# Optimization experiments

Hardware: AMD Instinct MI355X
Metric: run time of the kernel (lower is better)

The kernel has to match this reference:

```python
import jax, jax.numpy as jnp
import numpy as np

D_MODEL = 1024
NUM_HEADS = 16
D_HEAD = D_MODEL // NUM_HEADS
WINDOW = 512
N_GLOBAL = 1


def longformer_mask(seq_len):
    # sliding window |i-j| <= window//2, plus global rows/cols for first N_GLOBAL tokens
    i = jnp.arange(seq_len)[:, None]
    j = jnp.arange(seq_len)[None, :]
    allowed = (jnp.abs(i - j) <= WINDOW // 2) | (i < N_GLOBAL) | (j < N_GLOBAL)
    return jnp.where(allowed, 0.0, -jnp.inf).astype(jnp.float32)


def setup_inputs() -> dict:
    key = jax.random.key(0)
    ks = jax.random.split(key, 6)
    B, S = 2, 2048
    scale = 1.0 / np.sqrt(D_MODEL)
    return {
        "hidden_states": jax.random.normal(ks[0], (B, S, D_MODEL), dtype=jnp.float32),
        "Wq": jax.random.normal(ks[1], (D_MODEL, D_MODEL), dtype=jnp.float32) * scale,
        "Wk": jax.random.normal(ks[2], (D_MODEL, D_MODEL), dtype=jnp.float32) * scale,
        "Wv": jax.random.normal(ks[3], (D_MODEL, D_MODEL), dtype=jnp.float32) * scale,
        "Wo": jax.random.normal(ks[4], (D_MODEL, D_MODEL), dtype=jnp.float32) * scale,
        "bo": jax.random.normal(ks[5], (D_MODEL,), dtype=jnp.float32) * 0.01,
    }


def reference(hidden_states, Wq, Wk, Wv, Wo, bo):
    B, S, _ = hidden_states.shape
    q = (hidden_states @ Wq).reshape(B, S, NUM_HEADS, D_HEAD).transpose(0, 2, 1, 3)
    k = (hidden_states @ Wk).reshape(B, S, NUM_HEADS, D_HEAD).transpose(0, 2, 1, 3)
    v = (hidden_states @ Wv).reshape(B, S, NUM_HEADS, D_HEAD).transpose(0, 2, 1, 3)
    mask = longformer_mask(S)  # [S, S]
    scores = jnp.einsum('bhqd,bhkd->bhqk', q, k) / np.sqrt(D_HEAD)
    scores = scores + mask[None, None]
    attn = jax.nn.softmax(scores, axis=-1)
    out = jnp.einsum('bhqk,bhkd->bhqd', attn, v)
    out = out.transpose(0, 2, 1, 3).reshape(B, S, D_MODEL)
    return out @ Wo + bo
```

## Files before the change

### kernel.cpp

```cpp
#include <hip/hip_runtime.h>
#include <cstdint>
#include <cstddef>

#define DM 1024
#define NH 16
#define DH 64
#define SEQ 2048
#define NB 2
#define WIN2 256
#define QBLK 64
#define KBLK 128

typedef float f32x4 __attribute__((ext_vector_type(4)));
typedef __bf16 bf16x8 __attribute__((ext_vector_type(8)));
typedef unsigned short u16x8 __attribute__((ext_vector_type(8)));
typedef unsigned short u16x4 __attribute__((ext_vector_type(4)));
typedef float f32x4v __attribute__((ext_vector_type(4)));

__device__ __forceinline__ unsigned short f2bf(float x) {
  unsigned int u = __float_as_uint(x);
  u += 0x7FFFu + ((u >> 16) & 1u);
  return (unsigned short)(u >> 16);
}
__device__ __forceinline__ float bf2f(unsigned short h) {
  return __uint_as_float(((unsigned int)h) << 16);
}
__device__ __forceinline__ f32x4 mfma_bf16(u16x8 a, u16x8 b, f32x4 c) {
  return __builtin_amdgcn_mfma_f32_16x16x32_bf16(
      __builtin_bit_cast(bf16x8, a), __builtin_bit_cast(bf16x8, b), c, 0, 0, 0);
}

__global__ __launch_bounds__(256) void hsplit_kernel(
    const float* __restrict__ x, unsigned short* __restrict__ hi,
    unsigned short* __restrict__ lo, int n4) {
  int i = blockIdx.x * 256 + threadIdx.x;
  int stride = gridDim.x * 256;
  for (; i < n4; i += stride) {
    f32x4v v = *(const f32x4v*)(x + (size_t)i * 4);
    u16x4 h, l;
#pragma unroll
    for (int j = 0; j < 4; ++j) {
      h[j] = f2bf(v[j]);
      l[j] = f2bf(v[j] - bf2f(h[j]));
    }
    *(u16x4*)(hi + (size_t)i * 4) = h;
    *(u16x4*)(lo + (size_t)i * 4) = l;
  }
}

__global__ __launch_bounds__(256) void wsplit_kernel(
    const float* __restrict__ W0, const float* __restrict__ W1,
    const float* __restrict__ W2, const float* __restrict__ W3,
    unsigned short* __restrict__ pwhi, unsigned short* __restrict__ pwlo) {
  __shared__ float tile[32][33];
  const float* W = blockIdx.z == 0 ? W0 : blockIdx.z == 1 ? W1 : blockIdx.z == 2 ? W2 : W3;
  unsigned short* ohi = pwhi + (size_t)blockIdx.z * DM * DM;
  unsigned short* olo = pwlo + (size_t)blockIdx.z * DM * DM;
  int k0 = blockIdx.y * 32, n0 = blockIdx.x * 32;
  int c = threadIdx.x & 31, r0 = threadIdx.x >> 5;
#pragma unroll
  for (int i = 0; i < 4; ++i) {
    int r = r0 + i * 8;
    tile[r][c] = W[(size_t)(k0 + r) * DM + n0 + c];
  }
  __syncthreads();
#pragma unroll
  for (int i = 0; i < 4; ++i) {
    int nr = r0 + i * 8;
    float v = tile[c][nr];
    unsigned short h = f2bf(v);
    unsigned short l = f2bf(v - bf2f(h));
    ohi[(size_t)(n0 + nr) * DM + k0 + c] = h;
    olo[(size_t)(n0 + nr) * DM + k0 + c] = l;
  }
}

template <int MODE>
__global__ __launch_bounds__(256) void gemm_split_kernel(
    const unsigned short* __restrict__ Ahi, const unsigned short* __restrict__ Alo,
    const unsigned short* __restrict__ Wthi, const unsigned short* __restrict__ Wtlo,
    unsigned short* __restrict__ Qo, unsigned short* __restrict__ Ko,
    unsigned short* __restrict__ Vo, float* __restrict__ Out,
    const float* __restrict__ bias) {
  __shared__ alignas(16) unsigned short sAh[128][40];
  __shared__ alignas(16) unsigned short sAl[128][40];
  __shared__ alignas(16) unsigned short sBh[128][40];
  __shared__ alignas(16) unsigned short sBl[128][40];
  const int t = threadIdx.x;
  const int lane = t & 63, wave = t >> 6;
  const int l15 = lane & 15, l4 = lane >> 4;
  const int wr = wave >> 1, wc = wave & 1;
  const int mB = blockIdx.y, nB = blockIdx.x, wz = blockIdx.z;
  const unsigned short* Bh = Wthi + (size_t)(MODE == 0 ? wz : 3) * DM * DM;
  const unsigned short* Bl = Wtlo + (size_t)(MODE == 0 ? wz : 3) * DM * DM;
  f32x4 acc[4][4];
#pragma unroll
  for (int m = 0; m < 4; ++m)
#pragma unroll
    for (int n = 0; n < 4; ++n) acc[m][n] = (f32x4)0.0f;

  for (int kt = 0; kt < DM / 32; ++kt) {
    __syncthreads();
#pragma unroll
    for (int i = 0; i < 2; ++i) {
      int slot = t + i * 256;
      int row = slot >> 2, c8 = slot & 3;
      size_t ga = (size_t)(mB * 128 + row) * DM + kt * 32 + c8 * 8;
      *(u16x8*)&sAh[row][c8 * 8] = *(const u16x8*)(Ahi + ga);
      *(u16x8*)&sAl[row][c8 * 8] = *(const u16x8*)(Alo + ga);
      size_t gb = (size_t)(nB * 128 + row) * DM + kt * 32 + c8 * 8;
      *(u16x8*)&sBh[row][c8 * 8] = *(const u16x8*)(Bh + gb);
      *(u16x8*)&sBl[row][c8 * 8] = *(const u16x8*)(Bl + gb);
    }
    __syncthreads();
    u16x8 ah[4], al[4];
#pragma unroll
    for (int m = 0; m < 4; ++m) {
      ah[m] = *(const u16x8*)&sAh[wr * 64 + m * 16 + l15][8 * l4];
      al[m] = *(const u16x8*)&sAl[wr * 64 + m * 16 + l15][8 * l4];
    }
#pragma unroll
    for (int n = 0; n < 4; ++n) {
      u16x8 bh = *(const u16x8*)&sBh[wc * 64 + n * 16 + l15][8 * l4];
      u16x8 bl = *(const u16x8*)&sBl[wc * 64 + n * 16 + l15][8 * l4];
#pragma unroll
      for (int m = 0; m < 4; ++m) {
        acc[m][n] = mfma_bf16(ah[m], bh, acc[m][n]);
        acc[m][n] = mfma_bf16(ah[m], bl, acc[m][n]);
        acc[m][n] = mfma_bf16(al[m], bh, acc[m][n]);
      }
    }
  }
#pragma unroll
  for (int m = 0; m < 4; ++m)
#pragma unroll
    for (int n = 0; n < 4; ++n)
#pragma unroll
      for (int r = 0; r < 4; ++r) {
        int rg = mB * 128 + wr * 64 + m * 16 + l4 * 4 + r;
        int cg = nB * 128 + wc * 64 + n * 16 + l15;
        float v = acc[m][n][r];
        if constexpr (MODE == 0) {
          int b = rg >> 11, s = rg & 2047, h = cg >> 6, d = cg & 63;
          unsigned short bf = f2bf(v);
          if (wz == 0) {
            Qo[((size_t)((b << 4) + h) * SEQ + s) * DH + d] = bf;
          } else if (wz == 1) {
            Ko[((size_t)((b << 4) + h) * SEQ + s) * DH + d] = bf;
          } else {
            Vo[((size_t)((b << 4) + h) * DH + d) * SEQ + s] = bf;
          }
        } else {
          Out[(size_t)rg * DM + cg] = v + bias[cg];
        }
      }
}

__global__ __launch_bounds__(256) void attn_kernel(
    const unsigned short* __restrict__ Qg, const unsigned short* __restrict__ Kg,
    const unsigned short* __restrict__ Vtg, unsigned short* __restrict__ Ohi,
    unsigned short* __restrict__ Olo) {
  __shared__ alignas(16) unsigned short sK[KBLK][72];
  __shared__ alignas(16) unsigned short sVt[DH][136];
  __shared__ alignas(16) unsigned short sP[QBLK][136];
  const int t = threadIdx.x;
  const int lane = t & 63, wave = t >> 6;
  const int l15 = lane & 15, l4 = lane >> 4;
  const int qb = blockIdx.x, h = blockIdx.y, b = blockIdx.z;
  const int q0 = qb * QBLK;
  const size_t hb = ((size_t)b * NH + h) * SEQ * DH;
  const int wrow = wave * 16;

  u16x8 qreg[2];
#pragma unroll
  for (int ks = 0; ks < 2; ++ks)
    qreg[ks] = *(const u16x8*)(Qg + hb + (size_t)(q0 + wrow + l15) * DH + ks * 32 + 8 * l4);

  f32x4 oacc[4];
#pragma unroll
  for (int n = 0; n < 4; ++n) oacc[n] = (f32x4)0.0f;
  float mrun[4], lrun[4];
#pragma unroll
  for (int r = 0; r < 4; ++r) { mrun[r] = -3.0e38f; lrun[r] = 0.0f; }

  const int tlo = (q0 >= WIN2) ? ((q0 - WIN2) >> 7) : 0;
  int thi = (q0 + QBLK - 1 + WIN2) >> 7;
  if (thi > SEQ / KBLK - 1) thi = SEQ / KBLK - 1;

  for (int tt = 0; tt < SEQ / KBLK; ++tt) {
    bool visit = (tt == 0) || (qb == 0) || (tt >= tlo && tt <= thi);
    if (!visit) continue;
    __syncthreads();
#pragma unroll
    for (int i = 0; i < 4; ++i) {
      int slot = t + i * 256;
      int row = slot >> 3, c8 = slot & 7;
      *(u16x8*)&sK[row][c8 * 8] =
          *(const u16x8*)(Kg + hb + (size_t)(tt * KBLK + row) * DH + c8 * 8);
    }
#pragma unroll
    for (int i = 0; i < 4; ++i) {
      int slot = t + i * 256;
      int d = slot >> 4, c16 = slot & 15;
      *(u16x8*)&sVt[d][c16 * 8] =
          *(const u16x8*)(Vtg + hb + (size_t)d * SEQ + tt * KBLK + c16 * 8);
    }
    __syncthreads();

    f32x4 sc[8];
#pragma unroll
    for (int n = 0; n < 8; ++n) sc[n] = (f32x4)0.0f;
#pragma unroll
    for (int ks = 0; ks < 2; ++ks) {
#pragma unroll
      for (int n = 0; n < 8; ++n) {
        u16x8 kb = *(const u16x8*)&sK[n * 16 + l15][ks * 32 + 8 * l4];
        sc[n] = mfma_bf16(qreg[ks], kb, sc[n]);
      }
    }
    const int iabs_base = q0 + wrow + l4 * 4;
    float tmax[4];
#pragma unroll
    for (int r = 0; r < 4; ++r) tmax[r] = -3.0e38f;
#pragma unroll
    for (int n = 0; n < 8; ++n) {
      int jabs = tt * KBLK + n * 16 + l15;
#pragma unroll
      for (int r = 0; r < 4; ++r) {
        int iabs = iabs_base + r;
        float s = sc[n][r] * 0.125f;
        int dd = iabs - jabs; if (dd < 0) dd = -dd;
        bool ok = (dd <= WIN2) || (iabs < 1) || (jabs < 1);
        s = ok ? s : -1.0e30f;
        sc[n][r] = s;
        tmax[r] = fmaxf(tmax[r], s);
      }
    }
#pragma unroll
    for (int r = 0; r < 4; ++r) {
      float v = tmax[r];
      v = fmaxf(v, __shfl_xor(v, 1));
      v = fmaxf(v, __shfl_xor(v, 2));
      v = fmaxf(v, __shfl_xor(v, 4));
      v = fmaxf(v, __shfl_xor(v, 8));
      tmax[r] = v;
    }
    float scl[4], tsum[4];
#pragma unroll
    for (int r = 0; r < 4; ++r) {
      float mnew = fmaxf(mrun[r], tmax[r]);
      scl[r] = __expf(mrun[r] - mnew);
      mrun[r] = mnew;
      tsum[r] = 0.0f;
    }
#pragma unroll
    for (int n = 0; n < 8; ++n) {
#pragma unroll
      for (int r = 0; r < 4; ++r) {
        float p = __expf(sc[n][r] - mrun[r]);
        sc[n][r] = p;
        tsum[r] += p;
      }
    }
#pragma unroll
    for (int r = 0; r < 4; ++r) {
      float v = tsum[r];
      v += __shfl_xor(v, 1);
      v += __shfl_xor(v, 2);
      v += __shfl_xor(v, 4);
      v += __shfl_xor(v, 8);
      lrun[r] = lrun[r] * scl[r] + v;
    }
#pragma unroll
    for (int n = 0; n < 4; ++n)
#pragma unroll
      for (int r = 0; r < 4; ++r) oacc[n][r] *= scl[r];
#pragma unroll
    for (int n = 0; n < 8; ++n)
#pragma unroll
      for (int r = 0; r < 4; ++r)
        sP[wrow + l4 * 4 + r][n * 16 + l15] = f2bf(sc[n][r]);
#pragma unroll
    for (int kt4 = 0; kt4 < 4; ++kt4) {
      u16x8 pa = *(const u16x8*)&sP[wrow + l15][kt4 * 32 + 8 * l4];
#pragma unroll
      for (int n = 0; n < 4; ++n) {
        u16x8 vb = *(const u16x8*)&sVt[n * 16 + l15][kt4 * 32 + 8 * l4];
        oacc[n] = mfma_bf16(pa, vb, oacc[n]);
      }
    }
  }
#pragma unroll
  for (int n = 0; n < 4; ++n)
#pragma unroll
    for (int r = 0; r < 4; ++r) {
      int srow = q0 + wrow + l4 * 4 + r;
      int d = n * 16 + l15;
      float v = oacc[n][r] / lrun[r];
      unsigned short uhi = f2bf(v);
      unsigned short ulo = f2bf(v - bf2f(uhi));
      size_t o = ((size_t)b * SEQ + srow) * DM + h * DH + d;
      Ohi[o] = uhi;
      Olo[o] = ulo;
    }
}

extern "C" void kernel_launch(void* const* d_in, const int* in_sizes, int n_in,
                              void* d_out, int out_size, void* d_ws, size_t ws_size,
                              hipStream_t stream) {
  const float* hid = (const float*)d_in[0];
  const float* Wq = (const float*)d_in[1];
  const float* Wk = (const float*)d_in[2];
  const float* Wv = (const float*)d_in[3];
  const float* Wo = (const float*)d_in[4];
  const float* bo = (const float*)d_in[5];
  float* out = (float*)d_out;

  const size_t HS = (size_t)NB * SEQ * DM;
  unsigned short* hhi = (unsigned short*)d_ws;
  unsigned short* hlo = hhi + HS;
  unsigned short* wthi = hlo + HS;
  unsigned short* wtlo = wthi + (size_t)4 * DM * DM;
  unsigned short* Qb = wtlo + (size_t)4 * DM * DM;
  unsigned short* Kb = Qb + HS;
  unsigned short* Vtb = Kb + HS;
  unsigned short* attn_hi = hhi;
  unsigned short* attn_lo = hlo;

  hsplit_kernel<<<dim3(2048), dim3(256), 0, stream>>>(hid, hhi, hlo, (int)(HS / 4));
  wsplit_kernel<<<dim3(32, 32, 4), dim3(256), 0, stream>>>(Wq, Wk, Wv, Wo, wthi, wtlo);
  gemm_split_kernel<0><<<dim3(8, 32, 3), dim3(256), 0, stream>>>(
      hhi, hlo, wthi, wtlo, Qb, Kb, Vtb, nullptr, nullptr);
  attn_kernel<<<dim3(SEQ / QBLK, NH, NB), dim3(256), 0, stream>>>(
      Qb, Kb, Vtb, attn_hi, attn_lo);
  gemm_split_kernel<1><<<dim3(8, 32, 1), dim3(256), 0, stream>>>(
      attn_hi, attn_lo, wthi, wtlo, nullptr, nullptr, nullptr, out, bo);
}
```

Baseline: 340.4 us.

## Prefetch K/V tiles into registers, enlarge query block, skip interior masking

Attention now uses 128-query blocks with 512 threads (8 waves), which halves how often each K/V tile is reloaded per query. The next K/V tile is loaded into registers while the current tile is computed, then written to LDS between barriers. Tile-range logic is simplified, the mask is computed only for tiles that touch the window edge, and softmax uses exp2 with the log2e factor folded into the scale. Larger blocks mean fewer workgroups and more wasted out-of-window work per block, plus higher register pressure from the prefetch buffers.

```diff
diff --git a/kernel.cpp b/kernel.cpp
--- a/kernel.cpp
+++ b/kernel.cpp
@@ -8,8 +8,9 @@
 #define SEQ 2048
 #define NB 2
 #define WIN2 256
-#define QBLK 64
+#define QBLK 128
 #define KBLK 128
+#define NTILES (SEQ / KBLK)
 
 typedef float f32x4 __attribute__((ext_vector_type(4)));
 typedef __bf16 bf16x8 __attribute__((ext_vector_type(8)));
@@ -156,7 +157,7 @@
       }
 }
 
-__global__ __launch_bounds__(256) void attn_kernel(
+__global__ __launch_bounds__(512, 4) void attn_kernel(
     const unsigned short* __restrict__ Qg, const unsigned short* __restrict__ Kg,
     const unsigned short* __restrict__ Vtg, unsigned short* __restrict__ Ohi,
     unsigned short* __restrict__ Olo) {
@@ -170,6 +171,7 @@
   const int q0 = qb * QBLK;
   const size_t hb = ((size_t)b * NH + h) * SEQ * DH;
   const int wrow = wave * 16;
+  const float SC = 0.125f * 1.44269504089f;
 
   u16x8 qreg[2];
 #pragma unroll
@@ -183,29 +185,39 @@
 #pragma unroll
   for (int r = 0; r < 4; ++r) { mrun[r] = -3.0e38f; lrun[r] = 0.0f; }
 
-  const int tlo = (q0 >= WIN2) ? ((q0 - WIN2) >> 7) : 0;
-  int thi = (q0 + QBLK - 1 + WIN2) >> 7;
-  if (thi > SEQ / KBLK - 1) thi = SEQ / KBLK - 1;
-
-  for (int tt = 0; tt < SEQ / KBLK; ++tt) {
-    bool visit = (tt == 0) || (qb == 0) || (tt >= tlo && tt <= thi);
-    if (!visit) continue;
-    __syncthreads();
-#pragma unroll
-    for (int i = 0; i < 4; ++i) {
-      int slot = t + i * 256;
-      int row = slot >> 3, c8 = slot & 7;
-      *(u16x8*)&sK[row][c8 * 8] =
-          *(const u16x8*)(Kg + hb + (size_t)(tt * KBLK + row) * DH + c8 * 8);
-    }
-#pragma unroll
-    for (int i = 0; i < 4; ++i) {
-      int slot = t + i * 256;
-      int d = slot >> 4, c16 = slot & 15;
-      *(u16x8*)&sVt[d][c16 * 8] =
-          *(const u16x8*)(Vtg + hb + (size_t)d * SEQ + tt * KBLK + c16 * 8);
-    }
-    __syncthreads();
+  const int tl = (qb == 0) ? 0 : ((q0 >= WIN2) ? ((q0 - WIN2) >> 7) : 0);
+  int th = (qb == 0) ? (NTILES - 1) : ((q0 + QBLK - 1 + WIN2) >> 7);
+  if (th > NTILES - 1) th = NTILES - 1;
+
+  u16x8 pk[2], pv[2];
+#define ATTN_ISSUE(TT)                                                             \
+  {                                                                                \
+    _Pragma("unroll") for (int i = 0; i < 2; ++i) {                                \
+      int slot = t + i * 512;                                                      \
+      pk[i] = *(const u16x8*)(Kg + hb + (size_t)((TT)*KBLK + (slot >> 3)) * DH +   \
+                              (slot & 7) * 8);                                     \
+      pv[i] = *(const u16x8*)(Vtg + hb + (size_t)(slot >> 4) * SEQ + (TT)*KBLK +   \
+                              (slot & 15) * 8);                                    \
+    }                                                                              \
+  }
+#define ATTN_WRITE_LDS()                                                           \
+  {                                                                                \
+    _Pragma("unroll") for (int i = 0; i < 2; ++i) {                                \
+      int slot = t + i * 512;                                                      \
+      *(u16x8*)&sK[slot >> 3][(slot & 7) * 8] = pk[i];                             \
+      *(u16x8*)&sVt[slot >> 4][(slot & 15) * 8] = pv[i];                           \
+    }                                                                              \
+  }
+
+  ATTN_ISSUE(0);
+  ATTN_WRITE_LDS();
+  __syncthreads();
+
+  int tt = 0;
+  while (true) {
+    int ntt = (tt == 0) ? ((tl >= 1) ? tl : 1) : (tt + 1);
+    if (ntt > th) ntt = -1;
+    if (ntt >= 0) ATTN_ISSUE(ntt);
 
     f32x4 sc[8];
 #pragma unroll
@@ -219,22 +231,36 @@
       }
     }
     const int iabs_base = q0 + wrow + l4 * 4;
+    const int J0 = tt * KBLK;
+    const bool needmask =
+        ((J0 + KBLK - 1) - (q0 + wrow) > WIN2) || ((q0 + wrow + 15) - J0 > WIN2);
     float tmax[4];
 #pragma unroll
     for (int r = 0; r < 4; ++r) tmax[r] = -3.0e38f;
-#pragma unroll
-    for (int n = 0; n < 8; ++n) {
-      int jabs = tt * KBLK + n * 16 + l15;
-#pragma unroll
-      for (int r = 0; r < 4; ++r) {
-        int iabs = iabs_base + r;
-        float s = sc[n][r] * 0.125f;
-        int dd = iabs - jabs; if (dd < 0) dd = -dd;
-        bool ok = (dd <= WIN2) || (iabs < 1) || (jabs < 1);
-        s = ok ? s : -1.0e30f;
-        sc[n][r] = s;
-        tmax[r] = fmaxf(tmax[r], s);
-      }
+    if (needmask) {
+#pragma unroll
+      for (int n = 0; n < 8; ++n) {
+        int jabs = J0 + n * 16 + l15;
+#pragma unroll
+        for (int r = 0; r < 4; ++r) {
+          int iabs = iabs_base + r;
+          float s = sc[n][r] * SC;
+          int dd = iabs - jabs; if (dd < 0) dd = -dd;
+          bool ok = (dd <= WIN2) || (iabs < 1) || (jabs < 1);
+          s = ok ? s : -1.0e30f;
+          sc[n][r] = s;
+          tmax[r] = fmaxf(tmax[r], s);
+        }
+      }
+    } else {
+#pragma unroll
+      for (int n = 0; n < 8; ++n)
+#pragma unroll
+        for (int r = 0; r < 4; ++r) {
+          float s = sc[n][r] * SC;
+          sc[n][r] = s;
+          tmax[r] = fmaxf(tmax[r], s);
+        }
     }
 #pragma unroll
     for (int r = 0; r < 4; ++r) {
@@ -249,7 +275,7 @@
 #pragma unroll
     for (int r = 0; r < 4; ++r) {
       float mnew = fmaxf(mrun[r], tmax[r]);
-      scl[r] = __expf(mrun[r] - mnew);
+      scl[r] = exp2f(mrun[r] - mnew);
       mrun[r] = mnew;
       tsum[r] = 0.0f;
     }
@@ -257,7 +283,7 @@
     for (int n = 0; n < 8; ++n) {
 #pragma unroll
       for (int r = 0; r < 4; ++r) {
-        float p = __expf(sc[n][r] - mrun[r]);
+        float p = exp2f(sc[n][r] - mrun[r]);
         sc[n][r] = p;
         tsum[r] += p;
       }
@@ -289,7 +315,14 @@
         oacc[n] = mfma_bf16(pa, vb, oacc[n]);
       }
     }
-  }
+
+    if (ntt < 0) break;
+    __syncthreads();
+    ATTN_WRITE_LDS();
+    __syncthreads();
+    tt = ntt;
+  }
+
 #pragma unroll
   for (int n = 0; n < 4; ++n)
 #pragma unroll
@@ -331,7 +364,7 @@
   wsplit_kernel<<<dim3(32, 32, 4), dim3(256), 0, stream>>>(Wq, Wk, Wv, Wo, wthi, wtlo);
   gemm_split_kernel<0><<<dim3(8, 32, 3), dim3(256), 0, stream>>>(
       hhi, hlo, wthi, wtlo, Qb, Kb, Vtb, nullptr, nullptr);
-  attn_kernel<<<dim3(SEQ / QBLK, NH, NB), dim3(256), 0, stream>>>(
+  attn_kernel<<<dim3(SEQ / QBLK, NH, NB), dim3(512), 0, stream>>>(
       Qb, Kb, Vtb, attn_hi, attn_lo);
   gemm_split_kernel<1><<<dim3(8, 32, 1), dim3(256), 0, stream>>>(
       attn_hi, attn_lo, wthi, wtlo, nullptr, nullptr, nullptr, out, bo);
```

New measurement: 369.4 us. 1.09x slower.
